# Optimization experiments

Hardware: AMD Instinct MI355X
Metric: run time of the kernel (lower is better)

## Reference

```python
import jax, jax.numpy as jnp
import numpy as np

FIELD_DIMS = [50000, 5000, 2000, 1000, 1000, 500, 300, 200]
OFFSETS = np.concatenate([[0], np.cumsum(FIELD_DIMS)[:-1]]).astype(np.int64)
INPUT_DIM = int(np.sum(FIELD_DIMS))  # 60000
NUM_FIELDS = len(FIELD_DIMS)         # 8
EMBED_DIM = 16
MLP_DIMS = [256, 128, 64]
BATCH = 2048


def _xavier(key, shape):
    fan_in, fan_out = shape[0], shape[1]
    bound = float(np.sqrt(6.0 / (fan_in + fan_out)))
    return jax.random.uniform(key, shape, jnp.float32, -bound, bound)


def setup_inputs() -> dict:
    key = jax.random.key(0)
    ks = jax.random.split(key, 16)
    # per-field indices in valid range
    cols = [jax.random.randint(jax.random.fold_in(ks[0], f), (BATCH,), 0, FIELD_DIMS[f], dtype=jnp.int64)
            for f in range(NUM_FIELDS)]
    x = jnp.stack(cols, axis=1)  # [B, F] int64
    emb_table = _xavier(ks[1], (INPUT_DIM, EMBED_DIM))  # concat of per-field nn.Embedding tables
    # FM linear: torch init uniform_(weight) in [0,1), zero bias
    w_lin = jax.random.uniform(ks[2], (INPUT_DIM,), jnp.float32)
    b_lin = jnp.zeros((), jnp.float32)
    dnn_in = NUM_FIELDS * EMBED_DIM  # 128
    w1 = _xavier(ks[3], (dnn_in, MLP_DIMS[0]));  b1 = jnp.zeros((MLP_DIMS[0],), jnp.float32)
    w2 = _xavier(ks[4], (MLP_DIMS[0], MLP_DIMS[1])); b2 = jnp.zeros((MLP_DIMS[1],), jnp.float32)
    w3 = _xavier(ks[5], (MLP_DIMS[1], MLP_DIMS[2])); b3 = jnp.zeros((MLP_DIMS[2],), jnp.float32)
    w_last = _xavier(ks[6], (MLP_DIMS[2], 1))  # no bias
    return {"x": x, "emb_table": emb_table, "w_lin": w_lin, "b_lin": b_lin,
            "w1": w1, "b1": b1, "w2": w2, "b2": b2, "w3": w3, "b3": b3, "w_last": w_last}


def reference(x, emb_table, w_lin, b_lin, w1, b1, w2, b2, w3, b3, w_last):
    B = x.shape[0]
    offsets = jnp.asarray(OFFSETS)
    x_off = x + offsets[None, :]                        # [B, F] global feature ids
    # embedding gathers (equivalent to per-field nn.Embedding on one concat table)
    dense_x = emb_table[x_off]                          # [B, F, D]
    # one-hot scatter + dense linear (faithful to original memory pattern)
    sparse_x = jnp.zeros((B, INPUT_DIM), jnp.float32).at[
        jnp.arange(B)[:, None], x_off].set(1.0)        # [B, input_dim]
    linear_out = sparse_x @ w_lin + b_lin               # [B]
    # FM second-order pooling
    square_of_sum = jnp.sum(dense_x, axis=1) ** 2       # [B, D]
    sum_of_square = jnp.sum(dense_x ** 2, axis=1)       # [B, D]
    fm_out = 0.5 * jnp.sum(square_of_sum - sum_of_square, axis=1)  # [B]
    y_fm = linear_out + fm_out
    # DNN component (dropout=0, no BN)
    h = dense_x.reshape(B, -1)                          # [B, F*D]
    h = jax.nn.relu(h @ w1 + b1)
    h = jax.nn.relu(h @ w2 + b2)
    h = jax.nn.relu(h @ w3 + b3)
    y_dnn = (h @ w_last)[:, 0]                          # [B]
    return y_fm + y_dnn
```

## Files before the change

### kernel.cpp

```cpp
#include <hip/hip_runtime.h>


#define NF   8
#define ED   16
#define IN0  128
#define N1   256
#define N2   128
#define N3   64
#define EPB  4
#define T    256

__device__ const int g_off[NF] = {0, 50000, 55000, 57000, 58000, 59000, 59500, 59800};

__global__ __launch_bounds__(T) void deepfm_fused(
    const int*   __restrict__ x,
    const float* __restrict__ emb,
    const float* __restrict__ wlin,
    const float* __restrict__ blin,
    const float* __restrict__ w1,
    const float* __restrict__ b1,
    const float* __restrict__ w2,
    const float* __restrict__ b2,
    const float* __restrict__ w3,
    const float* __restrict__ b3,
    const float* __restrict__ wlast,
    float*       __restrict__ out)
{
    __shared__ float h0[EPB][IN0];
    __shared__ float h1[EPB][N1];
    __shared__ float h2[EPB][N2];
    __shared__ float ps2[EPB][N2];
    __shared__ float ps3[3][EPB][N3];
    __shared__ float base[EPB];

    const int tid = threadIdx.x;
    const int b0  = blockIdx.x * EPB;

    {
        const int r = tid >> 6;
        const int f = (tid >> 3) & 7;
        const int p = tid & 7;
        const int idx = x[(b0 + r) * NF + f] + g_off[f];
        const float2 v = *(const float2*)(emb + idx * ED + p * 2);
        *(float2*)(&h0[r][f * ED + p * 2]) = v;
    }

    if (tid < 32) {
        const int r = tid >> 3, f = tid & 7;
        float lin = wlin[x[(b0 + r) * NF + f] + g_off[f]];
        lin += __shfl_xor(lin, 1);
        lin += __shfl_xor(lin, 2);
        lin += __shfl_xor(lin, 4);
        if ((tid & 7) == 0) base[r] = lin + blin[0];
    }
    __syncthreads();

    if (tid < 64) {
        const int r = tid >> 4, d = tid & 15;
        float s = 0.0f, ss = 0.0f;
        #pragma unroll
        for (int f = 0; f < NF; ++f) {
            const float v = h0[r][f * ED + d];
            s += v;
            ss = fmaf(v, v, ss);
        }
        float p = 0.5f * (s * s - ss);
        p += __shfl_xor(p, 1);
        p += __shfl_xor(p, 2);
        p += __shfl_xor(p, 4);
        p += __shfl_xor(p, 8);
        if (d == 0) base[r] += p;
    }

    {
        float acc[EPB];
        const float bb = b1[tid];
        #pragma unroll
        for (int e = 0; e < EPB; ++e) acc[e] = bb;

        #pragma unroll 4
        for (int k0 = 0; k0 < IN0; k0 += 4) {
            float4 hv[EPB];
            #pragma unroll
            for (int e = 0; e < EPB; ++e) hv[e] = *(const float4*)(&h0[e][k0]);
            #pragma unroll
            for (int i = 0; i < 4; ++i) {
                const float w = w1[(k0 + i) * N1 + tid];
                #pragma unroll
                for (int e = 0; e < EPB; ++e) {
                    const float hk = (i == 0) ? hv[e].x : (i == 1) ? hv[e].y
                                   : (i == 2) ? hv[e].z : hv[e].w;
                    acc[e] = fmaf(hk, w, acc[e]);
                }
            }
        }
        #pragma unroll
        for (int e = 0; e < EPB; ++e) h1[e][tid] = fmaxf(acc[e], 0.0f);
    }
    __syncthreads();

    {
        const int c     = tid & (N2 - 1);
        const int half  = tid >> 7;
        const int kbase = half * 128;
        float acc[EPB];
        #pragma unroll
        for (int e = 0; e < EPB; ++e) acc[e] = 0.0f;

        #pragma unroll 4
        for (int k0 = 0; k0 < 128; k0 += 4) {
            float4 hv[EPB];
            #pragma unroll
            for (int e = 0; e < EPB; ++e) hv[e] = *(const float4*)(&h1[e][kbase + k0]);
            #pragma unroll
            for (int i = 0; i < 4; ++i) {
                const float w = w2[(kbase + k0 + i) * N2 + c];
                #pragma unroll
                for (int e = 0; e < EPB; ++e) {
                    const float hk = (i == 0) ? hv[e].x : (i == 1) ? hv[e].y
                                   : (i == 2) ? hv[e].z : hv[e].w;
                    acc[e] = fmaf(hk, w, acc[e]);
                }
            }
        }
        if (half == 1) {
            #pragma unroll
            for (int e = 0; e < EPB; ++e) ps2[e][c] = acc[e];
        }
        __syncthreads();
        if (half == 0) {
            const float bb = b2[c];
            #pragma unroll
            for (int e = 0; e < EPB; ++e)
                h2[e][c] = fmaxf(acc[e] + ps2[e][c] + bb, 0.0f);
        }
    }
    __syncthreads();

    {
        const int c     = tid & (N3 - 1);
        const int seg   = tid >> 6;
        const int kbase = seg * 32;
        float acc[EPB];
        #pragma unroll
        for (int e = 0; e < EPB; ++e) acc[e] = 0.0f;

        #pragma unroll
        for (int k0 = 0; k0 < 32; k0 += 4) {
            float4 hv[EPB];
            #pragma unroll
            for (int e = 0; e < EPB; ++e) hv[e] = *(const float4*)(&h2[e][kbase + k0]);
            #pragma unroll
            for (int i = 0; i < 4; ++i) {
                const float w = w3[(kbase + k0 + i) * N3 + c];
                #pragma unroll
                for (int e = 0; e < EPB; ++e) {
                    const float hk = (i == 0) ? hv[e].x : (i == 1) ? hv[e].y
                                   : (i == 2) ? hv[e].z : hv[e].w;
                    acc[e] = fmaf(hk, w, acc[e]);
                }
            }
        }
        if (seg != 0) {
            #pragma unroll
            for (int e = 0; e < EPB; ++e) ps3[seg - 1][e][c] = acc[e];
        }
        __syncthreads();

        if (tid < 64) {
            const float bb = b3[c];
            const float wl = wlast[c];
            float t[EPB];
            #pragma unroll
            for (int e = 0; e < EPB; ++e) {
                const float v = acc[e] + ps3[0][e][c] + ps3[1][e][c] + ps3[2][e][c] + bb;
                t[e] = fmaxf(v, 0.0f) * wl;
            }
            #pragma unroll
            for (int off = 1; off < 64; off <<= 1) {
                #pragma unroll
                for (int e = 0; e < EPB; ++e) t[e] += __shfl_xor(t[e], off);
            }
            if (tid == 0) {
                #pragma unroll
                for (int e = 0; e < EPB; ++e) out[b0 + e] = base[e] + t[e];
            }
        }
    }
}

extern "C" void kernel_launch(void* const* d_in, const int* in_sizes, int n_in,
                              void* d_out, int out_size, void* d_ws, size_t ws_size,
                              hipStream_t stream) {
    const int*   x     = (const int*)d_in[0];
    const float* emb   = (const float*)d_in[1];
    const float* wlin  = (const float*)d_in[2];
    const float* blin  = (const float*)d_in[3];
    const float* w1    = (const float*)d_in[4];
    const float* b1    = (const float*)d_in[5];
    const float* w2    = (const float*)d_in[6];
    const float* b2    = (const float*)d_in[7];
    const float* w3    = (const float*)d_in[8];
    const float* b3    = (const float*)d_in[9];
    const float* wlast = (const float*)d_in[10];
    float* out = (float*)d_out;

    const int batch = in_sizes[0] / NF;
    dim3 grid(batch / EPB);
    deepfm_fused<<<grid, T, 0, stream>>>(x, emb, wlin, blin,
                                         w1, b1, w2, b2, w3, b3, wlast, out);
}
```

Before: 15.87 us.

## Double rows per block and split-K every MLP layer across 512 threads

Each block now handles 8 batch rows with 512 threads instead of 4 rows with 256, so each weight value loaded from global memory is reused across twice as many rows. All three dense layers use split-K: each thread computes two adjacent output columns over a K slice, and partial sums are combined through one shared scratch buffer reused by all layers. This cuts total weight traffic and keeps the per-thread loops short. In exchange there are extra shared-memory reductions and barriers, and the grid has half as many blocks, which may leave some compute units underused.

Measured after the change: 13.94 us. 1.14x faster.

```diff
diff --git a/kernel.cpp b/kernel.cpp
--- a/kernel.cpp
+++ b/kernel.cpp
@@ -7,8 +7,8 @@
 #define N1   256
 #define N2   128
 #define N3   64
-#define EPB  4
-#define T    256
+#define EPB  8
+#define T    512
 
 __device__ const int g_off[NF] = {0, 50000, 55000, 57000, 58000, 59000, 59500, 59800};
 
@@ -29,8 +29,7 @@
     __shared__ float h0[EPB][IN0];
     __shared__ float h1[EPB][N1];
     __shared__ float h2[EPB][N2];
-    __shared__ float ps2[EPB][N2];
-    __shared__ float ps3[3][EPB][N3];
+    __shared__ float ps[7 * EPB * N2];
     __shared__ float base[EPB];
 
     const int tid = threadIdx.x;
@@ -41,21 +40,20 @@
         const int f = (tid >> 3) & 7;
         const int p = tid & 7;
         const int idx = x[(b0 + r) * NF + f] + g_off[f];
-        const float2 v = *(const float2*)(emb + idx * ED + p * 2);
-        *(float2*)(&h0[r][f * ED + p * 2]) = v;
-    }
-
-    if (tid < 32) {
+        *(float2*)(&h0[r][f * ED + p * 2]) = *(const float2*)(emb + idx * ED + p * 2);
+    }
+
+    if (tid < 64) {
         const int r = tid >> 3, f = tid & 7;
         float lin = wlin[x[(b0 + r) * NF + f] + g_off[f]];
         lin += __shfl_xor(lin, 1);
         lin += __shfl_xor(lin, 2);
         lin += __shfl_xor(lin, 4);
-        if ((tid & 7) == 0) base[r] = lin + blin[0];
+        if (f == 0) base[r] = lin + blin[0];
     }
     __syncthreads();
 
-    if (tid < 64) {
+    if (tid < 128) {
         const int r = tid >> 4, d = tid & 15;
         float s = 0.0f, ss = 0.0f;
         #pragma unroll
@@ -73,19 +71,117 @@
     }
 
     {
+        const int c2    = (tid & 127) * 2;
+        const int seg   = tid >> 7;
+        const int kbase = seg * 32;
+        float2 acc[EPB];
+        const float2 bb = (seg == 0) ? *(const float2*)(b1 + c2) : make_float2(0.f, 0.f);
+        #pragma unroll
+        for (int e = 0; e < EPB; ++e) acc[e] = bb;
+
+        #pragma unroll 2
+        for (int k0 = 0; k0 < 32; k0 += 4) {
+            float4 hv[EPB];
+            #pragma unroll
+            for (int e = 0; e < EPB; ++e) hv[e] = *(const float4*)(&h0[e][kbase + k0]);
+            #pragma unroll
+            for (int i = 0; i < 4; ++i) {
+                const float2 w = *(const float2*)(w1 + (kbase + k0 + i) * N1 + c2);
+                #pragma unroll
+                for (int e = 0; e < EPB; ++e) {
+                    const float hk = (i == 0) ? hv[e].x : (i == 1) ? hv[e].y
+                                   : (i == 2) ? hv[e].z : hv[e].w;
+                    acc[e].x = fmaf(hk, w.x, acc[e].x);
+                    acc[e].y = fmaf(hk, w.y, acc[e].y);
+                }
+            }
+        }
+        if (seg != 0) {
+            #pragma unroll
+            for (int e = 0; e < EPB; ++e)
+                *(float2*)(&ps[(seg - 1) * (EPB * N1) + e * N1 + c2]) = acc[e];
+        }
+        __syncthreads();
+        if (seg == 0) {
+            #pragma unroll
+            for (int e = 0; e < EPB; ++e) {
+                float2 v = acc[e];
+                #pragma unroll
+                for (int s = 0; s < 3; ++s) {
+                    const float2 q = *(const float2*)(&ps[s * (EPB * N1) + e * N1 + c2]);
+                    v.x += q.x; v.y += q.y;
+                }
+                h1[e][c2]     = fmaxf(v.x, 0.0f);
+                h1[e][c2 + 1] = fmaxf(v.y, 0.0f);
+            }
+        }
+    }
+    __syncthreads();
+
+    {
+        const int c2    = (tid & 63) * 2;
+        const int seg   = tid >> 6;
+        const int kbase = seg * 32;
+        float2 acc[EPB];
+        #pragma unroll
+        for (int e = 0; e < EPB; ++e) acc[e] = make_float2(0.f, 0.f);
+
+        #pragma unroll 2
+        for (int k0 = 0; k0 < 32; k0 += 4) {
+            float4 hv[EPB];
+            #pragma unroll
+            for (int e = 0; e < EPB; ++e) hv[e] = *(const float4*)(&h1[e][kbase + k0]);
+            #pragma unroll
+            for (int i = 0; i < 4; ++i) {
+                const float2 w = *(const float2*)(w2 + (kbase + k0 + i) * N2 + c2);
+                #pragma unroll
+                for (int e = 0; e < EPB; ++e) {
+                    const float hk = (i == 0) ? hv[e].x : (i == 1) ? hv[e].y
+                                   : (i == 2) ? hv[e].z : hv[e].w;
+                    acc[e].x = fmaf(hk, w.x, acc[e].x);
+                    acc[e].y = fmaf(hk, w.y, acc[e].y);
+                }
+            }
+        }
+        if (seg != 0) {
+            #pragma unroll
+            for (int e = 0; e < EPB; ++e)
+                *(float2*)(&ps[(seg - 1) * (EPB * N2) + e * N2 + c2]) = acc[e];
+        }
+        __syncthreads();
+        if (seg == 0) {
+            const float2 bb = *(const float2*)(b2 + c2);
+            #pragma unroll
+            for (int e = 0; e < EPB; ++e) {
+                float2 v = acc[e];
+                #pragma unroll
+                for (int s = 0; s < 7; ++s) {
+                    const float2 q = *(const float2*)(&ps[s * (EPB * N2) + e * N2 + c2]);
+                    v.x += q.x; v.y += q.y;
+                }
+                h2[e][c2]     = fmaxf(v.x + bb.x, 0.0f);
+                h2[e][c2 + 1] = fmaxf(v.y + bb.y, 0.0f);
+            }
+        }
+    }
+    __syncthreads();
+
+    {
+        const int c     = tid & 63;
+        const int seg   = tid >> 6;
+        const int kbase = seg * 16;
         float acc[EPB];
-        const float bb = b1[tid];
-        #pragma unroll
-        for (int e = 0; e < EPB; ++e) acc[e] = bb;
-
-        #pragma unroll 4
-        for (int k0 = 0; k0 < IN0; k0 += 4) {
+        #pragma unroll
+        for (int e = 0; e < EPB; ++e) acc[e] = 0.0f;
+
+        #pragma unroll
+        for (int k0 = 0; k0 < 16; k0 += 4) {
             float4 hv[EPB];
             #pragma unroll
-            for (int e = 0; e < EPB; ++e) hv[e] = *(const float4*)(&h0[e][k0]);
+            for (int e = 0; e < EPB; ++e) hv[e] = *(const float4*)(&h2[e][kbase + k0]);
             #pragma unroll
             for (int i = 0; i < 4; ++i) {
-                const float w = w1[(k0 + i) * N1 + tid];
+                const float w = w3[(kbase + k0 + i) * N3 + c];
                 #pragma unroll
                 for (int e = 0; e < EPB; ++e) {
                     const float hk = (i == 0) ? hv[e].x : (i == 1) ? hv[e].y
@@ -94,76 +190,10 @@
                 }
             }
         }
-        #pragma unroll
-        for (int e = 0; e < EPB; ++e) h1[e][tid] = fmaxf(acc[e], 0.0f);
-    }
-    __syncthreads();
-
-    {
-        const int c     = tid & (N2 - 1);
-        const int half  = tid >> 7;
-        const int kbase = half * 128;
-        float acc[EPB];
-        #pragma unroll
-        for (int e = 0; e < EPB; ++e) acc[e] = 0.0f;
-
-        #pragma unroll 4
-        for (int k0 = 0; k0 < 128; k0 += 4) {
-            float4 hv[EPB];
-            #pragma unroll
-            for (int e = 0; e < EPB; ++e) hv[e] = *(const float4*)(&h1[e][kbase + k0]);
-            #pragma unroll
-            for (int i = 0; i < 4; ++i) {
-                const float w = w2[(kbase + k0 + i) * N2 + c];
-                #pragma unroll
-                for (int e = 0; e < EPB; ++e) {
-                    const float hk = (i == 0) ? hv[e].x : (i == 1) ? hv[e].y
-                                   : (i == 2) ? hv[e].z : hv[e].w;
-                    acc[e] = fmaf(hk, w, acc[e]);
-                }
-            }
-        }
-        if (half == 1) {
-            #pragma unroll
-            for (int e = 0; e < EPB; ++e) ps2[e][c] = acc[e];
-        }
-        __syncthreads();
-        if (half == 0) {
-            const float bb = b2[c];
+        if (seg != 0) {
             #pragma unroll
             for (int e = 0; e < EPB; ++e)
-                h2[e][c] = fmaxf(acc[e] + ps2[e][c] + bb, 0.0f);
-        }
-    }
-    __syncthreads();
-
-    {
-        const int c     = tid & (N3 - 1);
-        const int seg   = tid >> 6;
-        const int kbase = seg * 32;
-        float acc[EPB];
-        #pragma unroll
-        for (int e = 0; e < EPB; ++e) acc[e] = 0.0f;
-
-        #pragma unroll
-        for (int k0 = 0; k0 < 32; k0 += 4) {
-            float4 hv[EPB];
-            #pragma unroll
-            for (int e = 0; e < EPB; ++e) hv[e] = *(const float4*)(&h2[e][kbase + k0]);
-            #pragma unroll
-            for (int i = 0; i < 4; ++i) {
-                const float w = w3[(kbase + k0 + i) * N3 + c];
-                #pragma unroll
-                for (int e = 0; e < EPB; ++e) {
-                    const float hk = (i == 0) ? hv[e].x : (i == 1) ? hv[e].y
-                                   : (i == 2) ? hv[e].z : hv[e].w;
-                    acc[e] = fmaf(hk, w, acc[e]);
-                }
-            }
-        }
-        if (seg != 0) {
-            #pragma unroll
-            for (int e = 0; e < EPB; ++e) ps3[seg - 1][e][c] = acc[e];
+                ps[(seg - 1) * (EPB * N3) + e * N3 + c] = acc[e];
         }
         __syncthreads();
 
@@ -173,7 +203,9 @@
             float t[EPB];
             #pragma unroll
             for (int e = 0; e < EPB; ++e) {
-                const float v = acc[e] + ps3[0][e][c] + ps3[1][e][c] + ps3[2][e][c] + bb;
+                float v = acc[e] + bb;
+                #pragma unroll
+                for (int s = 0; s < 7; ++s) v += ps[s * (EPB * N3) + e * N3 + c];
                 t[e] = fmaxf(v, 0.0f) * wl;
             }
             #pragma unroll
```

## Register-double-buffer weight loads and remap MLP threads to 2x2 output tiles

Applied to the files above, without the earlier changes.

Restructures all three MLP layers so that each thread computes a 2-row by 2-column (or 2-row by 1-column) output tile. Weight chunks are prefetched into register buffers (wA/wB), so global weight loads for the next chunk overlap the FMAs on the current one. The first W1 chunk is issued before the embedding gather, hiding its latency behind the gather. The cost is heavy register use (64+ floats of buffers), and launch_bounds(T,2) is added to keep occupancy, which risks spills.

Result: slower. 24.40 us (+53.8%).

```diff
diff --git a/kernel.cpp b/kernel.cpp
--- a/kernel.cpp
+++ b/kernel.cpp
@@ -12,7 +12,11 @@
 
 __device__ const int g_off[NF] = {0, 50000, 55000, 57000, 58000, 59000, 59500, 59800};
 
-__global__ __launch_bounds__(T) void deepfm_fused(
+#define LOADW2(buf, wp, ldw, ch, CH) { \
+    _Pragma("unroll") for (int i_ = 0; i_ < (CH); ++i_) \
+        (buf)[i_] = *(const float2*)((wp) + ((ch) * (CH) + i_) * (ldw)); }
+
+__global__ __launch_bounds__(T, 2) void deepfm_fused(
     const int*   __restrict__ x,
     const float* __restrict__ emb,
     const float* __restrict__ wlin,
@@ -30,19 +34,25 @@
     __shared__ float h1[EPB][N1];
     __shared__ float h2[EPB][N2];
     __shared__ float ps2[EPB][N2];
-    __shared__ float ps3[3][EPB][N3];
+    __shared__ float ps3[2][EPB][N3];
     __shared__ float base[EPB];
 
     const int tid = threadIdx.x;
     const int b0  = blockIdx.x * EPB;
 
+    const int c2 = (tid & 127) * 2;
+    const int rg = tid >> 7;
+    const int r0 = rg * 2, r1 = rg * 2 + 1;
+    const float* w1p = w1 + c2;
+
+    float2 wA[32], wB[32];
+
+    LOADW2(wA, w1p, N1, 0, 32);
+
     {
-        const int r = tid >> 6;
-        const int f = (tid >> 3) & 7;
-        const int p = tid & 7;
+        const int r = tid >> 6, f = (tid >> 3) & 7, p = tid & 7;
         const int idx = x[(b0 + r) * NF + f] + g_off[f];
-        const float2 v = *(const float2*)(emb + idx * ED + p * 2);
-        *(float2*)(&h0[r][f * ED + p * 2]) = v;
+        *(float2*)(&h0[r][f * ED + p * 2]) = *(const float2*)(emb + idx * ED + p * 2);
     }
 
     if (tid < 32) {
@@ -51,8 +61,10 @@
         lin += __shfl_xor(lin, 1);
         lin += __shfl_xor(lin, 2);
         lin += __shfl_xor(lin, 4);
-        if ((tid & 7) == 0) base[r] = lin + blin[0];
-    }
+        if (f == 0) base[r] = lin + blin[0];
+    }
+
+    const float2 bb1 = *(const float2*)(b1 + c2);
     __syncthreads();
 
     if (tid < 64) {
@@ -72,119 +84,119 @@
         if (d == 0) base[r] += p;
     }
 
-    {
-        float acc[EPB];
-        const float bb = b1[tid];
+    float a00 = bb1.x, a01 = bb1.y, a10 = bb1.x, a11 = bb1.y;
+
+    #define FMAW1(buf, ch) { \
+        _Pragma("unroll") for (int i_ = 0; i_ < 32; i_ += 4) { \
+            const float4 ha = *(const float4*)(&h0[r0][(ch) * 32 + i_]); \
+            const float4 hb = *(const float4*)(&h0[r1][(ch) * 32 + i_]); \
+            _Pragma("unroll") for (int j_ = 0; j_ < 4; ++j_) { \
+                const float fa = ((const float*)&ha)[j_]; \
+                const float fb = ((const float*)&hb)[j_]; \
+                const float2 w = (buf)[i_ + j_]; \
+                a00 = fmaf(fa, w.x, a00); a01 = fmaf(fa, w.y, a01); \
+                a10 = fmaf(fb, w.x, a10); a11 = fmaf(fb, w.y, a11); } } }
+
+    LOADW2(wB, w1p, N1, 1, 32); FMAW1(wA, 0);
+    LOADW2(wA, w1p, N1, 2, 32); FMAW1(wB, 1);
+    LOADW2(wB, w1p, N1, 3, 32); FMAW1(wA, 2);
+    FMAW1(wB, 3);
+
+    *(float2*)(&h1[r0][c2]) = make_float2(fmaxf(a00, 0.f), fmaxf(a01, 0.f));
+    *(float2*)(&h1[r1][c2]) = make_float2(fmaxf(a10, 0.f), fmaxf(a11, 0.f));
+
+    const int c2b = (tid & 63) * 2;
+    const int rg2 = (tid >> 6) & 1;
+    const int kh  = tid >> 7;
+    const int r20 = rg2 * 2, r21 = rg2 * 2 + 1;
+    const float* w2p = w2 + kh * 128 * N2 + c2b;
+
+    LOADW2(wA, w2p, N2, 0, 32);
+    __syncthreads();
+
+    float b00 = 0.f, b01 = 0.f, b10 = 0.f, b11 = 0.f;
+
+    #define FMAW2(buf, ch) { \
+        _Pragma("unroll") for (int i_ = 0; i_ < 32; i_ += 4) { \
+            const float4 ha = *(const float4*)(&h1[r20][kh * 128 + (ch) * 32 + i_]); \
+            const float4 hb = *(const float4*)(&h1[r21][kh * 128 + (ch) * 32 + i_]); \
+            _Pragma("unroll") for (int j_ = 0; j_ < 4; ++j_) { \
+                const float fa = ((const float*)&ha)[j_]; \
+                const float fb = ((const float*)&hb)[j_]; \
+                const float2 w = (buf)[i_ + j_]; \
+                b00 = fmaf(fa, w.x, b00); b01 = fmaf(fa, w.y, b01); \
+                b10 = fmaf(fb, w.x, b10); b11 = fmaf(fb, w.y, b11); } } }
+
+    LOADW2(wB, w2p, N2, 1, 32); FMAW2(wA, 0);
+    LOADW2(wA, w2p, N2, 2, 32); FMAW2(wB, 1);
+    LOADW2(wB, w2p, N2, 3, 32); FMAW2(wA, 2);
+    FMAW2(wB, 3);
+
+    if (kh == 1) {
+        *(float2*)(&ps2[r20][c2b]) = make_float2(b00, b01);
+        *(float2*)(&ps2[r21][c2b]) = make_float2(b10, b11);
+    }
+    __syncthreads();
+    if (kh == 0) {
+        const float2 bb2 = *(const float2*)(b2 + c2b);
+        const float2 q0 = *(const float2*)(&ps2[r20][c2b]);
+        const float2 q1 = *(const float2*)(&ps2[r21][c2b]);
+        *(float2*)(&h2[r20][c2b]) = make_float2(fmaxf(b00 + q0.x + bb2.x, 0.f),
+                                                fmaxf(b01 + q0.y + bb2.y, 0.f));
+        *(float2*)(&h2[r21][c2b]) = make_float2(fmaxf(b10 + q1.x + bb2.x, 0.f),
+                                                fmaxf(b11 + q1.y + bb2.y, 0.f));
+    }
+
+    const int c3  = tid & 63;
+    const int rg3 = (tid >> 6) & 1;
+    const int kh3 = tid >> 7;
+    const int r30 = rg3 * 2, r31 = rg3 * 2 + 1;
+    const float* w3p = w3 + kh3 * 64 * N3 + c3;
+
+    float wsA[32], wsB[32];
+    #pragma unroll
+    for (int i_ = 0; i_ < 32; ++i_) wsA[i_] = w3p[i_ * N3];
+    __syncthreads();
+
+    float c0 = 0.f, c1 = 0.f;
+
+    #define FMAW3(buf, ch) { \
+        _Pragma("unroll") for (int i_ = 0; i_ < 32; i_ += 4) { \
+            const float4 ha = *(const float4*)(&h2[r30][kh3 * 64 + (ch) * 32 + i_]); \
+            const float4 hb = *(const float4*)(&h2[r31][kh3 * 64 + (ch) * 32 + i_]); \
+            _Pragma("unroll") for (int j_ = 0; j_ < 4; ++j_) { \
+                const float fa = ((const float*)&ha)[j_]; \
+                const float fb = ((const float*)&hb)[j_]; \
+                c0 = fmaf(fa, (buf)[i_ + j_], c0); \
+                c1 = fmaf(fb, (buf)[i_ + j_], c1); } } }
+
+    #pragma unroll
+    for (int i_ = 0; i_ < 32; ++i_) wsB[i_] = w3p[(32 + i_) * N3];
+    FMAW3(wsA, 0);
+    FMAW3(wsB, 1);
+
+    ps3[kh3][r30][c3] = c0;
+    ps3[kh3][r31][c3] = c1;
+    __syncthreads();
+
+    if (tid < 64) {
+        const int c = tid;
+        const float bb = b3[c];
+        const float wl = wlast[c];
+        float t[EPB];
         #pragma unroll
-        for (int e = 0; e < EPB; ++e) acc[e] = bb;
-
-        #pragma unroll 4
-        for (int k0 = 0; k0 < IN0; k0 += 4) {
-            float4 hv[EPB];
+        for (int r = 0; r < EPB; ++r) {
+            const float v = ps3[0][r][c] + ps3[1][r][c] + bb;
+            t[r] = fmaxf(v, 0.f) * wl;
+        }
+        #pragma unroll
+        for (int off = 1; off < 64; off <<= 1) {
             #pragma unroll
-            for (int e = 0; e < EPB; ++e) hv[e] = *(const float4*)(&h0[e][k0]);
+            for (int r = 0; r < EPB; ++r) t[r] += __shfl_xor(t[r], off);
+        }
+        if (tid == 0) {
             #pragma unroll
-            for (int i = 0; i < 4; ++i) {
-                const float w = w1[(k0 + i) * N1 + tid];
-                #pragma unroll
-                for (int e = 0; e < EPB; ++e) {
-                    const float hk = (i == 0) ? hv[e].x : (i == 1) ? hv[e].y
-                                   : (i == 2) ? hv[e].z : hv[e].w;
-                    acc[e] = fmaf(hk, w, acc[e]);
-                }
-            }
-        }
-        #pragma unroll
-        for (int e = 0; e < EPB; ++e) h1[e][tid] = fmaxf(acc[e], 0.0f);
-    }
-    __syncthreads();
-
-    {
-        const int c     = tid & (N2 - 1);
-        const int half  = tid >> 7;
-        const int kbase = half * 128;
-        float acc[EPB];
-        #pragma unroll
-        for (int e = 0; e < EPB; ++e) acc[e] = 0.0f;
-
-        #pragma unroll 4
-        for (int k0 = 0; k0 < 128; k0 += 4) {
-            float4 hv[EPB];
-            #pragma unroll
-            for (int e = 0; e < EPB; ++e) hv[e] = *(const float4*)(&h1[e][kbase + k0]);
-            #pragma unroll
-            for (int i = 0; i < 4; ++i) {
-                const float w = w2[(kbase + k0 + i) * N2 + c];
-                #pragma unroll
-                for (int e = 0; e < EPB; ++e) {
-                    const float hk = (i == 0) ? hv[e].x : (i == 1) ? hv[e].y
-                                   : (i == 2) ? hv[e].z : hv[e].w;
-                    acc[e] = fmaf(hk, w, acc[e]);
-                }
-            }
-        }
-        if (half == 1) {
-            #pragma unroll
-            for (int e = 0; e < EPB; ++e) ps2[e][c] = acc[e];
-        }
-        __syncthreads();
-        if (half == 0) {
-            const float bb = b2[c];
-            #pragma unroll
-            for (int e = 0; e < EPB; ++e)
-                h2[e][c] = fmaxf(acc[e] + ps2[e][c] + bb, 0.0f);
-        }
-    }
-    __syncthreads();
-
-    {
-        const int c     = tid & (N3 - 1);
-        const int seg   = tid >> 6;
-        const int kbase = seg * 32;
-        float acc[EPB];
-        #pragma unroll
-        for (int e = 0; e < EPB; ++e) acc[e] = 0.0f;
-
-        #pragma unroll
-        for (int k0 = 0; k0 < 32; k0 += 4) {
-            float4 hv[EPB];
-            #pragma unroll
-            for (int e = 0; e < EPB; ++e) hv[e] = *(const float4*)(&h2[e][kbase + k0]);
-            #pragma unroll
-            for (int i = 0; i < 4; ++i) {
-                const float w = w3[(kbase + k0 + i) * N3 + c];
-                #pragma unroll
-                for (int e = 0; e < EPB; ++e) {
-                    const float hk = (i == 0) ? hv[e].x : (i == 1) ? hv[e].y
-                                   : (i == 2) ? hv[e].z : hv[e].w;
-                    acc[e] = fmaf(hk, w, acc[e]);
-                }
-            }
-        }
-        if (seg != 0) {
-            #pragma unroll
-            for (int e = 0; e < EPB; ++e) ps3[seg - 1][e][c] = acc[e];
-        }
-        __syncthreads();
-
-        if (tid < 64) {
-            const float bb = b3[c];
-            const float wl = wlast[c];
-            float t[EPB];
-            #pragma unroll
-            for (int e = 0; e < EPB; ++e) {
-                const float v = acc[e] + ps3[0][e][c] + ps3[1][e][c] + ps3[2][e][c] + bb;
-                t[e] = fmaxf(v, 0.0f) * wl;
-            }
-            #pragma unroll
-            for (int off = 1; off < 64; off <<= 1) {
-                #pragma unroll
-                for (int e = 0; e < EPB; ++e) t[e] += __shfl_xor(t[e], off);
-            }
-            if (tid == 0) {
-                #pragma unroll
-                for (int e = 0; e < EPB; ++e) out[b0 + e] = base[e] + t[e];
-            }
+            for (int r = 0; r < EPB; ++r) out[b0 + r] = base[r] + t[r];
         }
     }
 }
```
